# Performance work log

Measured on AMD Instinct MI355X. Metric: run time of the kernel, lower is better.

The kernel has to match this reference:

```python
import jax, jax.numpy as jnp
import numpy as np

N, E, G, H, C = 50000, 500000, 128, 128, 2
DIMS = [(G, H), (H, 2 * H), (2 * H, H), (H, H // 2)]  # (F_in, F_out) per PNAConv


def _pna(x, src, dst, n, avg_log, Wpre, bpre, Wpost, bpost, Wlin, blin):
    # message: pre_nn(cat([x_i, x_j])) with x_i = target (dst), x_j = source (src)
    m = jnp.concatenate([x[dst], x[src]], axis=-1) @ Wpre + bpre  # [E, F_in]
    deg = jax.ops.segment_sum(jnp.ones((src.shape[0],), m.dtype), dst, num_segments=n)
    degc = jnp.maximum(deg, 1.0)[:, None]                          # clamp(1), as in PyG
    mean = jax.ops.segment_sum(m, dst, num_segments=n) / degc
    mean2 = jax.ops.segment_sum(m * m, dst, num_segments=n) / degc
    std = jnp.sqrt(jax.nn.relu(mean2 - mean * mean) + 1e-5)        # PyG StdAggregation
    has = (deg > 0)[:, None]
    mn = jnp.where(has, jax.ops.segment_min(m, dst, num_segments=n), 0.0)
    mx = jnp.where(has, jax.ops.segment_max(m, dst, num_segments=n), 0.0)
    agg = jnp.concatenate([mean, mn, mx, std], axis=-1)            # [N, 4*F_in]
    logd = jnp.log(degc + 1.0)
    out = jnp.concatenate([agg, agg * (logd / avg_log), agg * (avg_log / logd)], axis=-1)
    out = jnp.concatenate([x, out], axis=-1) @ Wpost + bpost       # [N, 13*F_in] -> [N, F_out]
    return out @ Wlin + blin


def _bn(x, gamma, beta):
    mu = jnp.mean(x, 0)
    var = jnp.mean((x - mu) ** 2, 0)  # biased, training-mode BatchNorm1d
    return gamma * (x - mu) * jax.lax.rsqrt(var + 1e-5) + beta


def _forward(edge_index, x,
             Wpre1, bpre1, Wpost1, bpost1, Wlin1, blin1, gamma1, beta1,
             Wpre2, bpre2, Wpost2, bpost2, Wlin2, blin2, gamma2, beta2,
             Wpre3, bpre3, Wpost3, bpost3, Wlin3, blin3, gamma3, beta3,
             Wpre4, bpre4, Wpost4, bpost4, Wlin4, blin4, gamma4, beta4,
             Wc, bc):
    src, dst = edge_index[0], edge_index[1]
    n = x.shape[0]
    both = jnp.concatenate([src, dst])
    deg_all = jax.ops.segment_sum(jnp.ones((both.shape[0],), x.dtype), both, num_segments=n)
    avg_log = jnp.mean(jnp.log(deg_all + 1.0))  # avg_deg['log'] scalar
    h1 = jax.nn.elu(_bn(_pna(x, src, dst, n, avg_log, Wpre1, bpre1, Wpost1, bpost1, Wlin1, blin1), gamma1, beta1))
    h2 = jax.nn.elu(_bn(_pna(h1, src, dst, n, avg_log, Wpre2, bpre2, Wpost2, bpost2, Wlin2, blin2), gamma2, beta2))
    h3 = jax.nn.elu(_bn(_pna(h2, src, dst, n, avg_log, Wpre3, bpre3, Wpost3, bpost3, Wlin3, blin3), gamma3, beta3))
    p4 = _pna(h3 + h1, src, dst, n, avg_log, Wpre4, bpre4, Wpost4, bpost4, Wlin4, blin4)
    b4 = _bn(p4, gamma4, beta4)
    h4 = jax.nn.elu(b4)
    return (h4 @ Wc + bc, p4, b4)


def setup_inputs() -> dict:
    key = jax.random.key(0)
    ks = jax.random.split(key, 40)
    k = iter(range(40))
    inp = {}
    inp["x"] = jax.random.normal(ks[next(k)], (N, G), jnp.float32)
    inp["edge_index"] = jax.random.randint(ks[next(k)], (2, E), 0, N, dtype=jnp.int32)
    for i, (fi, fo) in enumerate(DIMS, 1):
        inp[f"Wpre{i}"] = jax.random.normal(ks[next(k)], (2 * fi, fi), jnp.float32) / np.float32(np.sqrt(2 * fi))
        inp[f"bpre{i}"] = jnp.zeros((fi,), jnp.float32)
        inp[f"Wpost{i}"] = jax.random.normal(ks[next(k)], (13 * fi, fo), jnp.float32) / np.float32(np.sqrt(13 * fi))
        inp[f"bpost{i}"] = jnp.zeros((fo,), jnp.float32)
        inp[f"Wlin{i}"] = jax.random.normal(ks[next(k)], (fo, fo), jnp.float32) / np.float32(np.sqrt(fo))
        inp[f"blin{i}"] = jnp.zeros((fo,), jnp.float32)
        inp[f"gamma{i}"] = jnp.ones((fo,), jnp.float32)
        inp[f"beta{i}"] = jnp.zeros((fo,), jnp.float32)
    inp["Wc"] = jax.random.normal(ks[next(k)], (H // 2, C), jnp.float32) / np.float32(np.sqrt(H // 2))
    inp["bc"] = jnp.zeros((C,), jnp.float32)
    return inp


def reference(x, edge_index,
              Wpre1, bpre1, Wpost1, bpost1, Wlin1, blin1, gamma1, beta1,
              Wpre2, bpre2, Wpost2, bpost2, Wlin2, blin2, gamma2, beta2,
              Wpre3, bpre3, Wpost3, bpost3, Wlin3, blin3, gamma3, beta3,
              Wpre4, bpre4, Wpost4, bpost4, Wlin4, blin4, gamma4, beta4,
              Wc, bc):
    return _forward(edge_index, x,
                    Wpre1, bpre1, Wpost1, bpost1, Wlin1, blin1, gamma1, beta1,
                    Wpre2, bpre2, Wpost2, bpost2, Wlin2, blin2, gamma2, beta2,
                    Wpre3, bpre3, Wpost3, bpost3, Wlin3, blin3, gamma3, beta3,
                    Wpre4, bpre4, Wpost4, bpost4, Wlin4, blin4, gamma4, beta4,
                    Wc, bc)
```

## Files before the change

kernel.cpp:

```cpp
#include <hip/hip_runtime.h>
#include <math.h>

#define N_NODES 50000
#define N_EDGES 500000
#define SCAN_NB ((N_NODES + 1023) / 1024)

using bf16x8 = __attribute__((ext_vector_type(8))) short;
using f32x4  = __attribute__((ext_vector_type(4))) float;

__device__ inline float b2f(unsigned short u) {
  union { unsigned int i; float f; } v; v.i = ((unsigned int)u) << 16; return v.f;
}
__device__ inline unsigned short f2b(float f) {
  union { float f; unsigned int i; } v; v.f = f;
  unsigned int x = v.i;
  return (unsigned short)((x + 0x7fffu + ((x >> 16) & 1u)) >> 16);
}
__device__ inline unsigned int pk2(float a, float b) {
  return (unsigned int)f2b(a) | ((unsigned int)f2b(b) << 16);
}
__device__ inline void stv(unsigned short* p, float v) { *p = f2b(v); }
__device__ inline void stv(float* p, float v) { *p = v; }
__device__ inline float ldf(unsigned short u) { return b2f(u); }
__device__ inline float ldf(float f) { return f; }
__host__ __device__ inline int imin(int a, int b) { return a < b ? a : b; }

__device__ inline void gload16(const unsigned short* g, unsigned short* l) {
  __builtin_amdgcn_global_load_lds((const __attribute__((address_space(1))) unsigned int*)g,
                                   (__attribute__((address_space(3))) unsigned int*)l, 16, 0, 0);
}

__global__ void k_count(const int* __restrict__ src, const int* __restrict__ dst,
                        int* __restrict__ cnt, int* __restrict__ degall) {
  int e = blockIdx.x * blockDim.x + threadIdx.x;
  if (e < N_EDGES) {
    atomicAdd(&cnt[dst[e]], 1);
    atomicAdd(&degall[src[e]], 1);
    atomicAdd(&degall[dst[e]], 1);
  }
}

__global__ __launch_bounds__(1024) void k_scan1(const int* __restrict__ cnt, int* __restrict__ ptr,
                                                int* __restrict__ sums) {
  __shared__ int buf[1024];
  int i = blockIdx.x * 1024 + threadIdx.x;
  int v = (i < N_NODES) ? cnt[i] : 0;
  buf[threadIdx.x] = v;
  __syncthreads();
  for (int off = 1; off < 1024; off <<= 1) {
    int tv = (threadIdx.x >= off) ? buf[threadIdx.x - off] : 0;
    __syncthreads();
    buf[threadIdx.x] += tv;
    __syncthreads();
  }
  if (i < N_NODES) ptr[i] = buf[threadIdx.x] - v;
  if (threadIdx.x == 1023) sums[blockIdx.x] = buf[1023];
}

__global__ void k_scan2(int* __restrict__ sums) {
  if (threadIdx.x == 0) {
    int acc = 0;
    for (int b = 0; b < SCAN_NB; b++) {
      int t = sums[b];
      sums[b] = acc;
      acc += t;
    }
    sums[SCAN_NB] = acc;
  }
}

__global__ __launch_bounds__(1024) void k_scan3(int* __restrict__ ptr, const int* __restrict__ sums) {
  int i = blockIdx.x * 1024 + threadIdx.x;
  if (i < N_NODES) ptr[i] += sums[blockIdx.x];
  if (blockIdx.x == 0 && threadIdx.x == 0) ptr[N_NODES] = sums[SCAN_NB];
}

__global__ void k_fill(const int* __restrict__ src, const int* __restrict__ dst,
                       const int* __restrict__ ptr, int* __restrict__ cnt, int* __restrict__ col) {
  int e = blockIdx.x * blockDim.x + threadIdx.x;
  if (e < N_EDGES) {
    int d = dst[e];
    int pos = atomicAdd(&cnt[d], 1);
    col[ptr[d] + pos] = src[e];
  }
}

__global__ void k_avglog(const int* __restrict__ degall, float* __restrict__ scal) {
  __shared__ float L[256];
  float s = 0.f;
  for (int n = blockIdx.x * blockDim.x + threadIdx.x; n < N_NODES; n += gridDim.x * blockDim.x)
    s += logf((float)degall[n] + 1.0f);
  L[threadIdx.x] = s;
  __syncthreads();
  for (int o = 128; o > 0; o >>= 1) {
    if (threadIdx.x < o) L[threadIdx.x] += L[threadIdx.x + o];
    __syncthreads();
  }
  if (threadIdx.x == 0) atomicAdd(&scal[0], L[0]);
}

__global__ void k_avg_fin(float* scal) {
  float avg = scal[0] / (float)N_NODES;
  scal[1] = avg;
  scal[2] = 1.0f / avg;
}

__global__ void k_scalars(const int* __restrict__ ptr, const float* __restrict__ scal,
                          float* __restrict__ a_arr, float* __restrict__ c_arr) {
  int n = blockIdx.x * blockDim.x + threadIdx.x;
  if (n < N_NODES) {
    int d = ptr[n + 1] - ptr[n];
    float degc = fmaxf((float)d, 1.f);
    float logd = logf(degc + 1.f);
    a_arr[n] = logd * scal[2];
    c_arr[n] = scal[1] / logd;
  }
}

__global__ void k_cast(const float* __restrict__ x, unsigned short* __restrict__ xb, int total) {
  int i = blockIdx.x * blockDim.x + threadIdx.x;
  if (i < total) xb[i] = f2b(x[i]);
}

__global__ void k_tcast_pre(const float* __restrict__ Wpre, unsigned short* __restrict__ out, int F) {
  int i = blockIdx.x * blockDim.x + threadIdx.x;
  if (i < 2 * F * F) {
    int j = i / F, k = i % F;
    float v = (j < F) ? Wpre[(size_t)k * F + j] : Wpre[(size_t)(F + k) * F + (j - F)];
    out[i] = f2b(v);
  }
}

__global__ void k_biaspre(const float* __restrict__ bpre, float* __restrict__ biasPre, int F) {
  int j = threadIdx.x;
  if (j < 2 * F) biasPre[j] = (j < F) ? bpre[j] : 0.f;
}

__global__ __launch_bounds__(256) void k_wcombT(const float* __restrict__ A, const float* __restrict__ B,
                                                unsigned short* __restrict__ CT, int M, int Ncol, int K) {
  __shared__ float As[16][136];
  __shared__ float Bs[16][128];
  int tid = threadIdx.x;
  int row0 = blockIdx.y * 128, col0 = blockIdx.x * 128;
  int am = tid >> 1, ah = (tid & 1) * 8;
  int ty = tid >> 4, tx = tid & 15;
  float acc[8][8];
#pragma unroll
  for (int i = 0; i < 8; i++)
#pragma unroll
    for (int j = 0; j < 8; j++) acc[i][j] = 0.f;
  int arow = row0 + am;
  bool av = arow < M;
  const float* Ar = A + (size_t)arow * K;
  for (int k0 = 0; k0 < K; k0 += 16) {
    float4 a0 = make_float4(0, 0, 0, 0), a1 = make_float4(0, 0, 0, 0);
    if (av) {
      a0 = *(const float4*)(Ar + k0 + ah);
      a1 = *(const float4*)(Ar + k0 + ah + 4);
    }
    As[ah + 0][am] = a0.x; As[ah + 1][am] = a0.y; As[ah + 2][am] = a0.z; As[ah + 3][am] = a0.w;
    As[ah + 4][am] = a1.x; As[ah + 5][am] = a1.y; As[ah + 6][am] = a1.z; As[ah + 7][am] = a1.w;
#pragma unroll
    for (int i = 0; i < 2; i++) {
      int q = tid * 2 + i;
      int kk = q >> 5, j4 = (q & 31) * 4;
      int bc = col0 + j4;
      float4 b = make_float4(0, 0, 0, 0);
      if (bc < Ncol && (k0 + kk) < K) b = *(const float4*)(B + (size_t)(k0 + kk) * Ncol + bc);
      *(float4*)(&Bs[kk][j4]) = b;
    }
    __syncthreads();
#pragma unroll
    for (int kk = 0; kk < 16; kk++) {
      float av8[8], bv8[8];
#pragma unroll
      for (int i = 0; i < 8; i++) av8[i] = As[kk][ty * 8 + i];
#pragma unroll
      for (int j = 0; j < 8; j++) bv8[j] = Bs[kk][tx * 8 + j];
#pragma unroll
      for (int i = 0; i < 8; i++)
#pragma unroll
        for (int j = 0; j < 8; j++) acc[i][j] = fmaf(av8[i], bv8[j], acc[i][j]);
    }
    __syncthreads();
  }
#pragma unroll
  for (int i = 0; i < 8; i++) {
    int r = row0 + ty * 8 + i;
    if (r < M) {
#pragma unroll
      for (int j = 0; j < 8; j++) {
        int c = col0 + tx * 8 + j;
        if (c < Ncol) CT[(size_t)c * M + r] = f2b(acc[i][j]);
      }
    }
  }
}

template <typename To>
__global__ __launch_bounds__(256) void k_mm(
    const unsigned short* __restrict__ A, int K,
    const unsigned short* __restrict__ BT,
    const float* __restrict__ bias,
    To* __restrict__ C, int n0, int M, int Ncol) {
  __shared__ unsigned short lds[2][2][4096];
  const int tid = threadIdx.x;
  const int lane = tid & 63;
  const int wid = tid >> 6;
  const int wr = wid >> 1, wc = wid & 1;
  const int row0 = blockIdx.y * 128;
  const int col0 = blockIdx.x * 128;
  const int l15 = lane & 15, lq = lane >> 4;
  const int srow = wid * 32 + (lane >> 2);
  const int scol = (lane & 3) * 8;
  const unsigned short* gA0 = A + (size_t)imin(row0 + srow, N_NODES - 1) * K + scol;
  const unsigned short* gA1 = A + (size_t)imin(row0 + srow + 16, N_NODES - 1) * K + scol;
  const unsigned short* gB0 = BT + (size_t)(col0 + srow) * K + scol;
  const unsigned short* gB1 = BT + (size_t)(col0 + srow + 16) * K + scol;

  f32x4 acc[4][4];
#pragma unroll
  for (int m = 0; m < 4; m++)
#pragma unroll
    for (int n = 0; n < 4; n++) acc[m][n] = (f32x4){0.f, 0.f, 0.f, 0.f};

  auto stage = [&](int buf, int k0) {
    gload16(gA0 + k0, &lds[buf][0][wid * 1024]);
    gload16(gA1 + k0, &lds[buf][0][wid * 1024 + 512]);
    gload16(gB0 + k0, &lds[buf][1][wid * 1024]);
    gload16(gB1 + k0, &lds[buf][1][wid * 1024 + 512]);
  };

  const int nk = K / 32;
  stage(0, 0);
  __syncthreads();
  for (int t = 0; t < nk; ++t) {
    const int cur = t & 1;
    if (t + 1 < nk) stage(cur ^ 1, (t + 1) * 32);
    bf16x8 a[4], b[4];
#pragma unroll
    for (int m = 0; m < 4; m++)
      a[m] = *(const bf16x8*)&lds[cur][0][(wr * 64 + m * 16 + l15) * 32 + lq * 8];
#pragma unroll
    for (int n = 0; n < 4; n++)
      b[n] = *(const bf16x8*)&lds[cur][1][(wc * 64 + n * 16 + l15) * 32 + lq * 8];
#pragma unroll
    for (int m = 0; m < 4; m++)
#pragma unroll
      for (int n = 0; n < 4; n++)
        acc[m][n] = __builtin_amdgcn_mfma_f32_16x16x32_bf16(a[m], b[n], acc[m][n], 0, 0, 0);
    __syncthreads();
  }
#pragma unroll
  for (int n = 0; n < 4; n++) {
    int col = col0 + wc * 64 + n * 16 + l15;
    float bv = bias ? bias[col] : 0.f;
#pragma unroll
    for (int m = 0; m < 4; m++) {
#pragma unroll
      for (int j = 0; j < 4; j++) {
        int r = row0 + wr * 64 + m * 16 + lq * 4 + j;
        if (r < M) stv(&C[(size_t)(n0 + r) * Ncol + col], acc[m][n][j] + bv);
      }
    }
  }
}

template <int NTILE, typename To>
__global__ __launch_bounds__(256) void k_mmT(
    const unsigned short* __restrict__ A, int K, int Mbuf,
    const unsigned short* __restrict__ BT,
    const float* __restrict__ bias,
    To* __restrict__ C, int n0, int M, int Ncol) {
  constexpr int CB = NTILE / 32;
  constexpr int NF = NTILE / 32;
  __shared__ unsigned short lds[2][(64 + NTILE) * 64];
  const int tid = threadIdx.x;
  const int lane = tid & 63;
  const int wid = tid >> 6;
  const int wr = wid >> 1, wc = wid & 1;
  const int row0 = blockIdx.y * 64;
  const int col0 = blockIdx.x * NTILE;
  const int l15 = lane & 15, lq = lane >> 4;
  const int lr8 = lane >> 3;
  const int lc8 = lane & 7;

  f32x4 acc[2][NF];
#pragma unroll
  for (int m = 0; m < 2; m++)
#pragma unroll
    for (int n = 0; n < NF; n++) acc[m][n] = (f32x4){0.f, 0.f, 0.f, 0.f};

  auto stage = [&](int buf, int k0) {
    unsigned short* Ar = &lds[buf][0];
    unsigned short* Br = &lds[buf][64 * 64];
#pragma unroll
    for (int c = 0; c < 2; c++) {
      int r = (wid * 2 + c) * 8 + lr8;
      int gr = imin(row0 + r, Mbuf - 1);
      int gc = (lc8 ^ (r & 7)) * 8;
      gload16(A + (size_t)gr * K + k0 + gc, Ar + (wid * 2 + c) * 512);
    }
#pragma unroll
    for (int c = 0; c < CB; c++) {
      int r = (wid * CB + c) * 8 + lr8;
      int gc = (lc8 ^ (r & 7)) * 8;
      gload16(BT + (size_t)(col0 + r) * K + k0 + gc, Br + (wid * CB + c) * 512);
    }
  };

  const int nk = K / 64;
  stage(0, 0);
  __syncthreads();
  for (int t = 0; t < nk; ++t) {
    const int cur = t & 1;
    if (t + 1 < nk) stage(cur ^ 1, (t + 1) * 64);
    const unsigned short* Ar = &lds[cur][0];
    const unsigned short* Br = &lds[cur][64 * 64];
#pragma unroll
    for (int ks = 0; ks < 2; ks++) {
      bf16x8 a[2], b[NF];
#pragma unroll
      for (int m = 0; m < 2; m++) {
        int r = wr * 32 + m * 16 + l15;
        a[m] = *(const bf16x8*)&Ar[r * 64 + ((lq + ks * 4) ^ (r & 7)) * 8];
      }
#pragma unroll
      for (int n = 0; n < NF; n++) {
        int r = wc * (NTILE / 2) + n * 16 + l15;
        b[n] = *(const bf16x8*)&Br[r * 64 + ((lq + ks * 4) ^ (r & 7)) * 8];
      }
#pragma unroll
      for (int m = 0; m < 2; m++)
#pragma unroll
        for (int n = 0; n < NF; n++)
          acc[m][n] = __builtin_amdgcn_mfma_f32_16x16x32_bf16(a[m], b[n], acc[m][n], 0, 0, 0);
    }
    __syncthreads();
  }
#pragma unroll
  for (int n = 0; n < NF; n++) {
    int col = col0 + wc * (NTILE / 2) + n * 16 + l15;
    float bv = bias ? bias[col] : 0.f;
#pragma unroll
    for (int m = 0; m < 2; m++) {
#pragma unroll
      for (int j = 0; j < 4; j++) {
        int r = row0 + wr * 32 + m * 16 + lq * 4 + j;
        if (r < M) stv(&C[(size_t)(n0 + r) * Ncol + col], acc[m][n][j] + bv);
      }
    }
  }
}

template <int F>
__global__ __launch_bounds__(256) void k_edge_agg(
    const unsigned short* __restrict__ ts, const unsigned short* __restrict__ xin,
    const int* __restrict__ ptr, const int* __restrict__ col,
    const float* __restrict__ a_arr, const float* __restrict__ c_arr,
    unsigned short* __restrict__ aggx, int n0, int nchunk) {
  constexpr int VU = F / 128;
  int idx = (blockIdx.x * blockDim.x + threadIdx.x) >> 6;
  int lane = threadIdx.x & 63;
  if (idx >= nchunk) return;
  int n = n0 + idx;
  if (n >= N_NODES) return;
  float S1[2 * VU], S2[2 * VU], mn[2 * VU], mx[2 * VU];
#pragma unroll
  for (int u = 0; u < 2 * VU; u++) {
    S1[u] = 0.f; S2[u] = 0.f; mn[u] = 3.4e38f; mx[u] = -3.4e38f;
  }
  int e0 = ptr[n], e1 = ptr[n + 1];
  for (int e = e0; e < e1; ++e) {
    int sidx = col[e];
    const unsigned int* sr = (const unsigned int*)(ts + (size_t)sidx * 2 * F + F);
#pragma unroll
    for (int u = 0; u < VU; u++) {
      unsigned int v = sr[lane + 64 * u];
      float f0 = b2f((unsigned short)(v & 0xffff));
      float f1 = b2f((unsigned short)(v >> 16));
      S1[2 * u] += f0; S2[2 * u] += f0 * f0;
      mn[2 * u] = fminf(mn[2 * u], f0); mx[2 * u] = fmaxf(mx[2 * u], f0);
      S1[2 * u + 1] += f1; S2[2 * u + 1] += f1 * f1;
      mn[2 * u + 1] = fminf(mn[2 * u + 1], f1); mx[2 * u + 1] = fmaxf(mx[2 * u + 1], f1);
    }
  }
  int d = e1 - e0;
  float an = a_arr[n], cn = c_arr[n];
  const unsigned int* tr = (const unsigned int*)(ts + (size_t)n * 2 * F);
  const unsigned int* xr = (const unsigned int*)(xin + (size_t)n * F);
  unsigned int* ob = (unsigned int*)(aggx + (size_t)idx * 13 * F);
  constexpr int UB = 64 * VU;
#pragma unroll
  for (int u = 0; u < VU; u++) {
    int ui = lane + 64 * u;
    ob[ui] = xr[ui];
    float mean0, mean1, lo0, lo1, hi0, hi1, sd0, sd1;
    if (d > 0) {
      float inv = 1.f / (float)d;
      unsigned int tv = tr[ui];
      float t0 = b2f((unsigned short)(tv & 0xffff));
      float t1 = b2f((unsigned short)(tv >> 16));
      float ms0 = S1[2 * u] * inv, ms1 = S1[2 * u + 1] * inv;
      sd0 = sqrtf(fmaxf(S2[2 * u] * inv - ms0 * ms0, 0.f) + 1e-5f);
      sd1 = sqrtf(fmaxf(S2[2 * u + 1] * inv - ms1 * ms1, 0.f) + 1e-5f);
      mean0 = t0 + ms0; mean1 = t1 + ms1;
      lo0 = t0 + mn[2 * u]; lo1 = t1 + mn[2 * u + 1];
      hi0 = t0 + mx[2 * u]; hi1 = t1 + mx[2 * u + 1];
    } else {
      mean0 = mean1 = lo0 = lo1 = hi0 = hi1 = 0.f;
      sd0 = sd1 = sqrtf(1e-5f);
    }
    unsigned int* o1 = ob + UB + ui;
    o1[0] = pk2(mean0, mean1);
    o1[UB] = pk2(lo0, lo1);
    o1[2 * UB] = pk2(hi0, hi1);
    o1[3 * UB] = pk2(sd0, sd1);
    o1[4 * UB] = pk2(an * mean0, an * mean1);
    o1[5 * UB] = pk2(an * lo0, an * lo1);
    o1[6 * UB] = pk2(an * hi0, an * hi1);
    o1[7 * UB] = pk2(an * sd0, an * sd1);
    o1[8 * UB] = pk2(cn * mean0, cn * mean1);
    o1[9 * UB] = pk2(cn * lo0, cn * lo1);
    o1[10 * UB] = pk2(cn * hi0, cn * hi1);
    o1[11 * UB] = pk2(cn * sd0, cn * sd1);
  }
}

template <int FO>
__global__ __launch_bounds__(256) void k_bn_stats_bf(const unsigned short* __restrict__ o,
                                                     float* __restrict__ gsum, float* __restrict__ gsq) {
  constexpr int TOTAL = N_NODES * FO;
  float s1[8], s2[8];
#pragma unroll
  for (int j = 0; j < 8; j++) { s1[j] = 0.f; s2[j] = 0.f; }
  const int stride = gridDim.x * 2048;
  for (int base = blockIdx.x * 2048 + threadIdx.x * 8; base < TOTAL; base += stride) {
    uint4 v = *(const uint4*)(o + base);
    const unsigned int* u = (const unsigned int*)&v;
#pragma unroll
    for (int w = 0; w < 4; w++) {
      float f0 = b2f((unsigned short)(u[w] & 0xffff));
      float f1 = b2f((unsigned short)(u[w] >> 16));
      s1[2 * w] += f0; s2[2 * w] += f0 * f0;
      s1[2 * w + 1] += f1; s2[2 * w + 1] += f1 * f1;
    }
  }
  __shared__ float L1[2048], L2[2048];
#pragma unroll
  for (int j = 0; j < 8; j++) {
    L1[threadIdx.x * 8 + j] = s1[j];
    L2[threadIdx.x * 8 + j] = s2[j];
  }
  __syncthreads();
  int c = threadIdx.x;
  if (c < FO) {
    float a1 = 0.f, a2 = 0.f;
    for (int i = c; i < 2048; i += FO) { a1 += L1[i]; a2 += L2[i]; }
    atomicAdd(&gsum[c], a1);
    atomicAdd(&gsq[c], a2);
  }
}

template <int FO>
__global__ __launch_bounds__(256) void k_bn_stats_f32(const float* __restrict__ o,
                                                      float* __restrict__ gsum, float* __restrict__ gsq) {
  constexpr int TOTAL = N_NODES * FO;
  float s1[4], s2[4];
#pragma unroll
  for (int j = 0; j < 4; j++) { s1[j] = 0.f; s2[j] = 0.f; }
  const int stride = gridDim.x * 1024;
  for (int base = blockIdx.x * 1024 + threadIdx.x * 4; base < TOTAL; base += stride) {
    float4 v = *(const float4*)(o + base);
    s1[0] += v.x; s2[0] += v.x * v.x;
    s1[1] += v.y; s2[1] += v.y * v.y;
    s1[2] += v.z; s2[2] += v.z * v.z;
    s1[3] += v.w; s2[3] += v.w * v.w;
  }
  __shared__ float L1[1024], L2[1024];
#pragma unroll
  for (int j = 0; j < 4; j++) {
    L1[threadIdx.x * 4 + j] = s1[j];
    L2[threadIdx.x * 4 + j] = s2[j];
  }
  __syncthreads();
  int c = threadIdx.x;
  if (c < FO) {
    float a1 = 0.f, a2 = 0.f;
    for (int i = c; i < 1024; i += FO) { a1 += L1[i]; a2 += L2[i]; }
    atomicAdd(&gsum[c], a1);
    atomicAdd(&gsq[c], a2);
  }
}

__global__ void k_bn_fin(const float* bnsum, const float* bnsq, float* bnmean, float* bnrs, int FO) {
  int c = threadIdx.x;
  if (c < FO) {
    float mean = bnsum[c] / (float)N_NODES;
    float var = bnsq[c] / (float)N_NODES - mean * mean;
    bnmean[c] = mean;
    bnrs[c] = rsqrtf(var + 1e-5f);
  }
}

template <int FO>
__global__ __launch_bounds__(256) void k_bn_elu_bf(const unsigned short* __restrict__ o,
                                                   const float* __restrict__ mean, const float* __restrict__ rs,
                                                   const float* __restrict__ gamma, const float* __restrict__ beta,
                                                   unsigned short* __restrict__ h) {
  constexpr int TOTAL = N_NODES * FO;
  int base = (blockIdx.x * blockDim.x + threadIdx.x) * 8;
  if (base >= TOTAL) return;
  int c0 = base % FO;
  uint4 v = *(const uint4*)(o + base);
  const unsigned int* u = (const unsigned int*)&v;
  unsigned int outw[4];
#pragma unroll
  for (int w = 0; w < 4; w++) {
    int c = c0 + 2 * w;
    float f0 = b2f((unsigned short)(u[w] & 0xffff));
    float f1 = b2f((unsigned short)(u[w] >> 16));
    float y0 = gamma[c] * (f0 - mean[c]) * rs[c] + beta[c];
    float y1 = gamma[c + 1] * (f1 - mean[c + 1]) * rs[c + 1] + beta[c + 1];
    y0 = y0 > 0.f ? y0 : expm1f(y0);
    y1 = y1 > 0.f ? y1 : expm1f(y1);
    outw[w] = pk2(y0, y1);
  }
  *(uint4*)(h + base) = *(uint4*)outw;
}

template <int FO>
__global__ __launch_bounds__(256) void k_bn_elu_f32(const float* __restrict__ o,
                                                    const float* __restrict__ mean, const float* __restrict__ rs,
                                                    const float* __restrict__ gamma, const float* __restrict__ beta,
                                                    unsigned short* __restrict__ h, float* __restrict__ bnout) {
  constexpr int TOTAL = N_NODES * FO;
  int base = (blockIdx.x * blockDim.x + threadIdx.x) * 4;
  if (base >= TOTAL) return;
  int c = base % FO;
  float4 v = *(const float4*)(o + base);
  float y0 = gamma[c] * (v.x - mean[c]) * rs[c] + beta[c];
  float y1 = gamma[c + 1] * (v.y - mean[c + 1]) * rs[c + 1] + beta[c + 1];
  float y2 = gamma[c + 2] * (v.z - mean[c + 2]) * rs[c + 2] + beta[c + 2];
  float y3 = gamma[c + 3] * (v.w - mean[c + 3]) * rs[c + 3] + beta[c + 3];
  if (bnout) *(float4*)(bnout + base) = make_float4(y0, y1, y2, y3);
  unsigned int o0 = pk2(y0 > 0.f ? y0 : expm1f(y0), y1 > 0.f ? y1 : expm1f(y1));
  unsigned int o1 = pk2(y2 > 0.f ? y2 : expm1f(y2), y3 > 0.f ? y3 : expm1f(y3));
  *(uint2*)(h + base) = make_uint2(o0, o1);
}

__global__ void k_bcomb(const float* __restrict__ bpost, const float* __restrict__ Wlin,
                        const float* __restrict__ blin, float* __restrict__ bcomb, int FO) {
  int j = threadIdx.x;
  if (j < FO) {
    float acc = blin[j];
    for (int k = 0; k < FO; k++) acc += bpost[k] * Wlin[k * FO + j];
    bcomb[j] = acc;
  }
}

__global__ void k_add(const unsigned short* __restrict__ a, const unsigned short* __restrict__ b,
                      unsigned short* __restrict__ c) {
  int idx = blockIdx.x * blockDim.x + threadIdx.x;
  if (idx < N_NODES * 128) c[idx] = f2b(b2f(a[idx]) + b2f(b[idx]));
}

__global__ void k_logits(const unsigned short* __restrict__ h4, const float* __restrict__ Wc,
                         const float* __restrict__ bc, float* __restrict__ out) {
  int n = blockIdx.x * blockDim.x + threadIdx.x;
  if (n < N_NODES) {
    float acc0 = bc[0], acc1 = bc[1];
    const unsigned short* hr = h4 + (size_t)n * 64;
    for (int k = 0; k < 64; k++) {
      float v = b2f(hr[k]);
      acc0 += v * Wc[k * 2 + 0];
      acc1 += v * Wc[k * 2 + 1];
    }
    out[n * 2 + 0] = acc0;
    out[n * 2 + 1] = acc1;
  }
}

struct WS {
  int *ptr, *col, *cnt, *degall, *scansums;
  float *scal, *a_arr, *c_arr, *bnsum, *bnsq, *bnmean, *bnrs, *bcomb, *biasPre;
  unsigned short *wcombT, *wpreT;
  unsigned short *xb, *h1, *h2, *h3, *ts, *aggx;
  size_t agg_elems;
};

template <int F, typename To>
static void run_layer(const unsigned short* xin, To* o_ptr, float* bnout, unsigned short* hout,
                      const float* Wpre, const float* bpre, const float* Wpost, const float* bpost,
                      const float* Wlin, const float* blin, const float* gamma, const float* beta,
                      int FO, const WS& ws, hipStream_t stream) {
  const int N = N_NODES;
  const int K13 = 13 * F;
  {
    dim3 g((FO + 127) / 128, (K13 + 127) / 128);
    k_wcombT<<<g, 256, 0, stream>>>(Wpost, Wlin, ws.wcombT, K13, FO, FO);
    k_bcomb<<<1, 256, 0, stream>>>(bpost, Wlin, blin, ws.bcomb, FO);
    k_tcast_pre<<<(2 * F * F + 255) / 256, 256, 0, stream>>>(Wpre, ws.wpreT, F);
    k_biaspre<<<1, 512, 0, stream>>>(bpre, ws.biasPre, F);
  }
  {
    dim3 g(2 * F / 128, (N + 127) / 128);
    k_mm<unsigned short><<<g, 256, 0, stream>>>(xin, F, ws.wpreT, ws.biasPre, ws.ts, 0, N, 2 * F);
  }
  int NB = (int)(ws.agg_elems / (size_t)K13);
  NB &= ~127;
  if (NB > N) NB = N;
  if (NB < 128) NB = 128;
  for (int c0 = 0; c0 < N; c0 += NB) {
    int nc = (N - c0 < NB) ? (N - c0) : NB;
    k_edge_agg<F><<<(nc + 3) / 4, 256, 0, stream>>>(ws.ts, xin, ws.ptr, ws.col,
                                                    ws.a_arr, ws.c_arr, ws.aggx, c0, nc);
    if (FO == 64) {
      dim3 g(1, (nc + 63) / 64);
      k_mmT<64, To><<<g, 256, 0, stream>>>(ws.aggx, K13, NB, ws.wcombT, ws.bcomb, o_ptr, c0, nc, FO);
    } else {
      dim3 g(FO / 128, (nc + 63) / 64);
      k_mmT<128, To><<<g, 256, 0, stream>>>(ws.aggx, K13, NB, ws.wcombT, ws.bcomb, o_ptr, c0, nc, FO);
    }
  }
  hipMemsetAsync(ws.bnsum, 0, 512 * sizeof(float), stream);
  constexpr bool is_bf = (sizeof(To) == 2);
  if constexpr (is_bf) {
    int gs = imin((N * FO) / 2048 + 1, 1024);
    if (FO == 128)
      k_bn_stats_bf<128><<<gs, 256, 0, stream>>>((const unsigned short*)o_ptr, ws.bnsum, ws.bnsq);
    else
      k_bn_stats_bf<256><<<gs, 256, 0, stream>>>((const unsigned short*)o_ptr, ws.bnsum, ws.bnsq);
  } else {
    int gs = imin((N * FO) / 1024 + 1, 1024);
    k_bn_stats_f32<64><<<gs, 256, 0, stream>>>((const float*)o_ptr, ws.bnsum, ws.bnsq);
  }
  k_bn_fin<<<1, 256, 0, stream>>>(ws.bnsum, ws.bnsq, ws.bnmean, ws.bnrs, FO);
  int total = N_NODES * FO;
  if constexpr (is_bf) {
    int ge = (total / 8 + 255) / 256;
    if (FO == 128)
      k_bn_elu_bf<128><<<ge, 256, 0, stream>>>((const unsigned short*)o_ptr, ws.bnmean, ws.bnrs, gamma, beta, hout);
    else
      k_bn_elu_bf<256><<<ge, 256, 0, stream>>>((const unsigned short*)o_ptr, ws.bnmean, ws.bnrs, gamma, beta, hout);
  } else {
    int ge = (total / 4 + 255) / 256;
    k_bn_elu_f32<64><<<ge, 256, 0, stream>>>((const float*)o_ptr, ws.bnmean, ws.bnrs, gamma, beta, hout, bnout);
  }
}

extern "C" void kernel_launch(void* const* d_in, const int* in_sizes, int n_in,
                              void* d_out, int out_size, void* d_ws, size_t ws_size,
                              hipStream_t stream) {
  const int N = N_NODES, E = N_EDGES;
  const float* x = (const float*)d_in[0];
  const int* ei = (const int*)d_in[1];
  const int* src = ei;
  const int* dst = ei + E;
  const float *Wpre[4], *bpre[4], *Wpost[4], *bpost[4], *Wlin[4], *blin[4], *gamma[4], *beta[4];
  for (int i = 0; i < 4; i++) {
    const int b = 2 + i * 8;
    Wpre[i] = (const float*)d_in[b + 0];
    bpre[i] = (const float*)d_in[b + 1];
    Wpost[i] = (const float*)d_in[b + 2];
    bpost[i] = (const float*)d_in[b + 3];
    Wlin[i] = (const float*)d_in[b + 4];
    blin[i] = (const float*)d_in[b + 5];
    gamma[i] = (const float*)d_in[b + 6];
    beta[i] = (const float*)d_in[b + 7];
  }
  const float* Wc = (const float*)d_in[34];
  const float* bcv = (const float*)d_in[35];

  char* w = (char*)d_ws;
  size_t off = 0;
  auto alloc = [&](size_t bytes) -> void* {
    void* p = (void*)(w + off);
    off = (off + bytes + 255) & ~(size_t)255;
    return p;
  };
  WS ws;
  ws.ptr = (int*)alloc((N + 1) * sizeof(int));
  ws.col = (int*)alloc((size_t)E * sizeof(int));
  ws.cnt = (int*)alloc((size_t)N * sizeof(int));
  ws.degall = (int*)alloc((size_t)N * sizeof(int));
  ws.scansums = (int*)alloc((SCAN_NB + 1) * sizeof(int));
  ws.scal = (float*)alloc(16 * sizeof(float));
  ws.a_arr = (float*)alloc((size_t)N * sizeof(float));
  ws.c_arr = (float*)alloc((size_t)N * sizeof(float));
  ws.bnsum = (float*)alloc(256 * sizeof(float));
  ws.bnsq = (float*)alloc(256 * sizeof(float));
  ws.bnmean = (float*)alloc(256 * sizeof(float));
  ws.bnrs = (float*)alloc(256 * sizeof(float));
  ws.bcomb = (float*)alloc(256 * sizeof(float));
  ws.biasPre = (float*)alloc(512 * sizeof(float));
  ws.wcombT = (unsigned short*)alloc((size_t)256 * 3328 * sizeof(unsigned short));
  ws.wpreT = (unsigned short*)alloc((size_t)512 * 256 * sizeof(unsigned short));
  ws.xb = (unsigned short*)alloc((size_t)N * 128 * sizeof(unsigned short));
  ws.h1 = (unsigned short*)alloc((size_t)N * 128 * sizeof(unsigned short));
  ws.h2 = (unsigned short*)alloc((size_t)N * 256 * sizeof(unsigned short));
  ws.h3 = (unsigned short*)alloc((size_t)N * 128 * sizeof(unsigned short));
  ws.ts = (unsigned short*)alloc((size_t)N * 512 * sizeof(unsigned short));
  size_t rem = (ws_size > off) ? (ws_size - off) : 0;
  ws.agg_elems = rem / sizeof(unsigned short);
  ws.aggx = (unsigned short*)(w + off);
  unsigned short* h4 = ws.xb;

  float* outp = (float*)d_out;
  float* logits = outp;
  float* p4 = outp + (size_t)N * 2;
  float* b4 = p4 + (size_t)N * 64;
  unsigned short* o_scratch = (unsigned short*)p4;

  hipMemsetAsync(ws.cnt, 0, N * sizeof(int), stream);
  hipMemsetAsync(ws.degall, 0, N * sizeof(int), stream);
  hipMemsetAsync(ws.scal, 0, 16 * sizeof(float), stream);
  k_count<<<(E + 255) / 256, 256, 0, stream>>>(src, dst, ws.cnt, ws.degall);
  k_scan1<<<SCAN_NB, 1024, 0, stream>>>(ws.cnt, ws.ptr, ws.scansums);
  k_scan2<<<1, 64, 0, stream>>>(ws.scansums);
  k_scan3<<<SCAN_NB, 1024, 0, stream>>>(ws.ptr, ws.scansums);
  hipMemsetAsync(ws.cnt, 0, N * sizeof(int), stream);
  k_fill<<<(E + 255) / 256, 256, 0, stream>>>(src, dst, ws.ptr, ws.cnt, ws.col);
  k_avglog<<<64, 256, 0, stream>>>(ws.degall, ws.scal);
  k_avg_fin<<<1, 1, 0, stream>>>(ws.scal);
  k_scalars<<<(N + 255) / 256, 256, 0, stream>>>(ws.ptr, ws.scal, ws.a_arr, ws.c_arr);
  k_cast<<<(N * 128 + 255) / 256, 256, 0, stream>>>(x, ws.xb, N * 128);

  run_layer<128, unsigned short>(ws.xb, o_scratch, nullptr, ws.h1,
                                 Wpre[0], bpre[0], Wpost[0], bpost[0], Wlin[0], blin[0], gamma[0], beta[0],
                                 128, ws, stream);
  run_layer<128, unsigned short>(ws.h1, o_scratch, nullptr, ws.h2,
                                 Wpre[1], bpre[1], Wpost[1], bpost[1], Wlin[1], blin[1], gamma[1], beta[1],
                                 256, ws, stream);
  run_layer<256, unsigned short>(ws.h2, o_scratch, nullptr, ws.h3,
                                 Wpre[2], bpre[2], Wpost[2], bpost[2], Wlin[2], blin[2], gamma[2], beta[2],
                                 128, ws, stream);
  k_add<<<((N * 128) + 255) / 256, 256, 0, stream>>>(ws.h1, ws.h3, ws.h3);
  run_layer<128, float>(ws.h3, p4, b4, h4,
                        Wpre[3], bpre[3], Wpost[3], bpost[3], Wlin[3], blin[3], gamma[3], beta[3],
                        64, ws, stream);
  k_logits<<<(N + 255) / 256, 256, 0, stream>>>(h4, Wc, bcv, logits);
  (void)in_sizes; (void)n_in; (void)out_size; (void)ws_size;
}
```

Before: 1.346 ms.

## Apply degree scalers inside post-GEMM instead of materializing scaled aggregates

The edge aggregation kernel now writes only the four base aggregates (4F per node) instead of the full 13F concatenation with x and the amplification/attenuation copies. The post GEMM reads x directly, reuses the same 4F aggregate buffer for three K-ranges against different weight slices, and combines the partial accumulators as identity + a*amp + c*att per row. This cuts the intermediate write and read traffic by roughly two thirds and allows larger node chunks. In exchange it keeps extra accumulator registers, adds per-row scaler loads, and changes rounding, since scaling now happens in fp32 rather than before bf16 packing.

```diff
diff --git a/kernel.cpp b/kernel.cpp
--- a/kernel.cpp
+++ b/kernel.cpp
@@ -266,12 +266,16 @@
   }
 }
 
-template <int NTILE, typename To>
-__global__ __launch_bounds__(256) void k_mmT(
-    const unsigned short* __restrict__ A, int K, int Mbuf,
+template <int NTILE, int F, typename To>
+__global__ __launch_bounds__(256) void k_mmP(
+    const unsigned short* __restrict__ X,
+    const unsigned short* __restrict__ G,
+    const float* __restrict__ a_arr, const float* __restrict__ c_arr,
     const unsigned short* __restrict__ BT,
     const float* __restrict__ bias,
-    To* __restrict__ C, int n0, int M, int Ncol) {
+    To* __restrict__ C, int n0, int M, int Mbuf, int Ncol) {
+  constexpr int K13 = 13 * F;
+  constexpr int F4 = 4 * F;
   constexpr int CB = NTILE / 32;
   constexpr int NF = NTILE / 32;
   __shared__ unsigned short lds[2][(64 + NTILE) * 64];
@@ -285,11 +289,24 @@
   const int lr8 = lane >> 3;
   const int lc8 = lane & 7;
 
-  f32x4 acc[2][NF];
+  f32x4 anv[2], cnv[2];
 #pragma unroll
   for (int m = 0; m < 2; m++)
 #pragma unroll
-    for (int n = 0; n < NF; n++) acc[m][n] = (f32x4){0.f, 0.f, 0.f, 0.f};
+    for (int j = 0; j < 4; j++) {
+      int g = imin(n0 + row0 + wr * 32 + m * 16 + lq * 4 + j, N_NODES - 1);
+      anv[m][j] = a_arr[g];
+      cnv[m][j] = c_arr[g];
+    }
+
+  f32x4 master[2][NF], acc[2][NF];
+#pragma unroll
+  for (int m = 0; m < 2; m++)
+#pragma unroll
+    for (int n = 0; n < NF; n++) {
+      master[m][n] = (f32x4){0.f, 0.f, 0.f, 0.f};
+      acc[m][n] = (f32x4){0.f, 0.f, 0.f, 0.f};
+    }
 
   auto stage = [&](int buf, int k0) {
     unsigned short* Ar = &lds[buf][0];
@@ -297,22 +314,31 @@
 #pragma unroll
     for (int c = 0; c < 2; c++) {
       int r = (wid * 2 + c) * 8 + lr8;
-      int gr = imin(row0 + r, Mbuf - 1);
       int gc = (lc8 ^ (r & 7)) * 8;
-      gload16(A + (size_t)gr * K + k0 + gc, Ar + (wid * 2 + c) * 512);
+      const unsigned short* src;
+      if (k0 < F) {
+        src = X + (size_t)imin(n0 + row0 + r, N_NODES - 1) * F + k0 + gc;
+      } else {
+        int q = k0 - F;
+        int reg = q / F4;
+        int koff = q - reg * F4;
+        src = G + (size_t)imin(row0 + r, Mbuf - 1) * F4 + koff + gc;
+      }
+      gload16(src, Ar + (wid * 2 + c) * 512);
     }
 #pragma unroll
     for (int c = 0; c < CB; c++) {
       int r = (wid * CB + c) * 8 + lr8;
       int gc = (lc8 ^ (r & 7)) * 8;
-      gload16(BT + (size_t)(col0 + r) * K + k0 + gc, Br + (wid * CB + c) * 512);
+      gload16(BT + (size_t)(col0 + r) * K13 + k0 + gc, Br + (wid * CB + c) * 512);
     }
   };
 
-  const int nk = K / 64;
+  const int nk = K13 / 64;
   stage(0, 0);
   __syncthreads();
   for (int t = 0; t < nk; ++t) {
+    const int k0 = t * 64;
     const int cur = t & 1;
     if (t + 1 < nk) stage(cur ^ 1, (t + 1) * 64);
     const unsigned short* Ar = &lds[cur][0];
@@ -337,17 +363,38 @@
           acc[m][n] = __builtin_amdgcn_mfma_f32_16x16x32_bf16(a[m], b[n], acc[m][n], 0, 0, 0);
     }
     __syncthreads();
-  }
+    if (k0 + 64 == 5 * F) {
+#pragma unroll
+      for (int m = 0; m < 2; m++)
+#pragma unroll
+        for (int n = 0; n < NF; n++) {
+          master[m][n] = acc[m][n];
+          acc[m][n] = (f32x4){0.f, 0.f, 0.f, 0.f};
+        }
+    } else if (k0 + 64 == 9 * F) {
+#pragma unroll
+      for (int m = 0; m < 2; m++)
+#pragma unroll
+        for (int n = 0; n < NF; n++) {
+          master[m][n] += anv[m] * acc[m][n];
+          acc[m][n] = (f32x4){0.f, 0.f, 0.f, 0.f};
+        }
+    }
+  }
+#pragma unroll
+  for (int m = 0; m < 2; m++)
+#pragma unroll
+    for (int n = 0; n < NF; n++) master[m][n] += cnv[m] * acc[m][n];
 #pragma unroll
   for (int n = 0; n < NF; n++) {
     int col = col0 + wc * (NTILE / 2) + n * 16 + l15;
-    float bv = bias ? bias[col] : 0.f;
+    float bv = bias[col];
 #pragma unroll
     for (int m = 0; m < 2; m++) {
 #pragma unroll
       for (int j = 0; j < 4; j++) {
         int r = row0 + wr * 32 + m * 16 + lq * 4 + j;
-        if (r < M) stv(&C[(size_t)(n0 + r) * Ncol + col], acc[m][n][j] + bv);
+        if (r < M) stv(&C[(size_t)(n0 + r) * Ncol + col], master[m][n][j] + bv);
       }
     }
   }
@@ -355,10 +402,9 @@
 
 template <int F>
 __global__ __launch_bounds__(256) void k_edge_agg(
-    const unsigned short* __restrict__ ts, const unsigned short* __restrict__ xin,
+    const unsigned short* __restrict__ ts,
     const int* __restrict__ ptr, const int* __restrict__ col,
-    const float* __restrict__ a_arr, const float* __restrict__ c_arr,
-    unsigned short* __restrict__ aggx, int n0, int nchunk) {
+    unsigned short* __restrict__ aggc, int n0, int nchunk) {
   constexpr int VU = F / 128;
   int idx = (blockIdx.x * blockDim.x + threadIdx.x) >> 6;
   int lane = threadIdx.x & 63;
@@ -386,15 +432,12 @@
     }
   }
   int d = e1 - e0;
-  float an = a_arr[n], cn = c_arr[n];
   const unsigned int* tr = (const unsigned int*)(ts + (size_t)n * 2 * F);
-  const unsigned int* xr = (const unsigned int*)(xin + (size_t)n * F);
-  unsigned int* ob = (unsigned int*)(aggx + (size_t)idx * 13 * F);
+  unsigned int* ob = (unsigned int*)(aggc + (size_t)idx * 4 * F);
   constexpr int UB = 64 * VU;
 #pragma unroll
   for (int u = 0; u < VU; u++) {
     int ui = lane + 64 * u;
-    ob[ui] = xr[ui];
     float mean0, mean1, lo0, lo1, hi0, hi1, sd0, sd1;
     if (d > 0) {
       float inv = 1.f / (float)d;
@@ -411,19 +454,11 @@
       mean0 = mean1 = lo0 = lo1 = hi0 = hi1 = 0.f;
       sd0 = sd1 = sqrtf(1e-5f);
     }
-    unsigned int* o1 = ob + UB + ui;
+    unsigned int* o1 = ob + ui;
     o1[0] = pk2(mean0, mean1);
     o1[UB] = pk2(lo0, lo1);
     o1[2 * UB] = pk2(hi0, hi1);
     o1[3 * UB] = pk2(sd0, sd1);
-    o1[4 * UB] = pk2(an * mean0, an * mean1);
-    o1[5 * UB] = pk2(an * lo0, an * lo1);
-    o1[6 * UB] = pk2(an * hi0, an * hi1);
-    o1[7 * UB] = pk2(an * sd0, an * sd1);
-    o1[8 * UB] = pk2(cn * mean0, cn * mean1);
-    o1[9 * UB] = pk2(cn * lo0, cn * lo1);
-    o1[10 * UB] = pk2(cn * hi0, cn * hi1);
-    o1[11 * UB] = pk2(cn * sd0, cn * sd1);
   }
 }
 
@@ -607,20 +642,21 @@
     dim3 g(2 * F / 128, (N + 127) / 128);
     k_mm<unsigned short><<<g, 256, 0, stream>>>(xin, F, ws.wpreT, ws.biasPre, ws.ts, 0, N, 2 * F);
   }
-  int NB = (int)(ws.agg_elems / (size_t)K13);
+  int NB = (int)(ws.agg_elems / (size_t)(4 * F));
   NB &= ~127;
   if (NB > N) NB = N;
   if (NB < 128) NB = 128;
   for (int c0 = 0; c0 < N; c0 += NB) {
     int nc = (N - c0 < NB) ? (N - c0) : NB;
-    k_edge_agg<F><<<(nc + 3) / 4, 256, 0, stream>>>(ws.ts, xin, ws.ptr, ws.col,
-                                                    ws.a_arr, ws.c_arr, ws.aggx, c0, nc);
+    k_edge_agg<F><<<(nc + 3) / 4, 256, 0, stream>>>(ws.ts, ws.ptr, ws.col, ws.aggx, c0, nc);
     if (FO == 64) {
       dim3 g(1, (nc + 63) / 64);
-      k_mmT<64, To><<<g, 256, 0, stream>>>(ws.aggx, K13, NB, ws.wcombT, ws.bcomb, o_ptr, c0, nc, FO);
+      k_mmP<64, F, To><<<g, 256, 0, stream>>>(xin, ws.aggx, ws.a_arr, ws.c_arr, ws.wcombT,
+                                              ws.bcomb, o_ptr, c0, nc, NB, FO);
     } else {
       dim3 g(FO / 128, (nc + 63) / 64);
-      k_mmT<128, To><<<g, 256, 0, stream>>>(ws.aggx, K13, NB, ws.wcombT, ws.bcomb, o_ptr, c0, nc, FO);
+      k_mmP<128, F, To><<<g, 256, 0, stream>>>(xin, ws.aggx, ws.a_arr, ws.c_arr, ws.wcombT,
+                                               ws.bcomb, o_ptr, c0, nc, NB, FO);
     }
   }
   hipMemsetAsync(ws.bnsum, 0, 512 * sizeof(float), stream);
```

Result: faster. 1.193 ms (-11.3%).
